# Kernel tuning notes

Measured on AMD Instinct MI355X. Metric: run time of the kernel, lower is better.

The kernel has to match this reference:

```python
import jax, jax.numpy as jnp
import numpy as np

B, N, K = 64, 128, 12
D_ATOM, D_NBR, D_NEW = 256, 320, 256
H, DK = 8, 32  # D_NEW = H * DK
LN_EPS = 1e-5
NEG_INF = -1e9


def setup_inputs() -> dict:
    key = jax.random.key(0)
    ks = jax.random.split(key, 10)
    atom_feature = jax.random.normal(ks[0], (B, N, D_ATOM), jnp.float32)
    atom_neighbor_feature = jax.random.normal(ks[1], (B, N, K, D_NBR), jnp.float32)
    # valid-neighbor masks from random neighbor counts in [1, K]
    counts = jax.random.randint(ks[2], (B, N), 1, K + 1)
    valid = (jnp.arange(K)[None, None, :] < counts[:, :, None]).astype(jnp.float32)
    atom_attend_mask = valid[..., None]                      # (B,N,K,1), 1=real neighbor
    atom_softmax_mask = (1.0 - valid[..., None]) * NEG_INF   # (B,N,K,1), additive
    # parameters
    s = 1.0 / np.sqrt(D_ATOM)
    W_atom = jax.random.uniform(ks[3], (D_ATOM, D_NEW), jnp.float32, -s, s)
    b_atom = jnp.zeros((D_NEW,), jnp.float32)
    s2 = 1.0 / np.sqrt(D_NBR)
    W_nbr = jax.random.uniform(ks[4], (D_NBR, D_NEW), jnp.float32, -s2, s2)
    b_nbr = jnp.zeros((D_NEW,), jnp.float32)
    s3 = 1.0 / np.sqrt(DK)
    w_align = jax.random.uniform(ks[5], (DK, 1), jnp.float32, -s3, s3)
    b_align = jnp.zeros((1,), jnp.float32)
    ln_gamma = jnp.ones((D_NEW,), jnp.float32)
    ln_beta = jnp.zeros((D_NEW,), jnp.float32)
    return dict(atom_feature=atom_feature, atom_neighbor_feature=atom_neighbor_feature,
                atom_softmax_mask=atom_softmax_mask, atom_attend_mask=atom_attend_mask,
                W_atom=W_atom, b_atom=b_atom, W_nbr=W_nbr, b_nbr=b_nbr,
                w_align=w_align, b_align=b_align, ln_gamma=ln_gamma, ln_beta=ln_beta)


def reference(atom_feature, atom_neighbor_feature, atom_softmax_mask, atom_attend_mask,
              W_atom, b_atom, W_nbr, b_nbr, w_align, b_align, ln_gamma, ln_beta):
    # dropout is identity at eval time
    h = atom_feature @ W_atom + b_atom                    # (B,N,D_NEW)
    e = atom_neighbor_feature @ W_nbr + b_nbr             # (B,N,K,D_NEW)
    h = h.reshape(B, N, 1, H, DK)                         # broadcast over K
    e = e.reshape(B, N, K, H, DK)
    # GATv2: act(h_i + e_j) then per-head linear score
    feat = jax.nn.leaky_relu(h + e)                       # slope 0.01 == torch default
    score = feat @ w_align + b_align                      # (B,N,K,H,1)
    score = score + atom_softmax_mask[:, :, :, None, :]   # additive -inf on pad
    attn = jax.nn.softmax(score, axis=2)                  # softmax over neighbors K
    attn = attn * atom_attend_mask[:, :, :, None, :]
    ctx = jnp.sum(attn * e, axis=2).reshape(B, N, H * DK)  # (B,N,D_NEW)
    # LayerNorm
    mu = jnp.mean(ctx, axis=-1, keepdims=True)
    xc = ctx - mu
    var = jnp.mean(xc * xc, axis=-1, keepdims=True)
    return xc * jax.lax.rsqrt(var + LN_EPS) * ln_gamma + ln_beta
```

## Files before the change

### kernel.cpp

```cpp
#include <hip/hip_runtime.h>

#define KN 12
#define DNBR 320
#define DNEW 256
#define BN_TOT 8192
#define ATB 4
#define KTOT 576
#define NKS 18
#define AROWS 55
#define ASTR 584

typedef short bf8_t __attribute__((ext_vector_type(8)));
typedef float f32x4 __attribute__((ext_vector_type(4)));
typedef unsigned short us8 __attribute__((ext_vector_type(8)));
using u16 = unsigned short;
using u32 = unsigned int;

__device__ __forceinline__ u16 f2bf(float f) {
    u32 x = __float_as_uint(f);
    return (u16)((x + 0x7fffu + ((x >> 16) & 1u)) >> 16);
}

__device__ __forceinline__ us8 pack8(float4 a, float4 b) {
    us8 v;
    v[0] = f2bf(a.x); v[1] = f2bf(a.y); v[2] = f2bf(a.z); v[3] = f2bf(a.w);
    v[4] = f2bf(b.x); v[5] = f2bf(b.y); v[6] = f2bf(b.z); v[7] = f2bf(b.w);
    return v;
}

__global__ __launch_bounds__(256) void build_b2(
    const float* __restrict__ Wn, const float* __restrict__ Wa,
    u16* __restrict__ B2)
{
    int tile = blockIdx.x * 4 + (threadIdx.x >> 6);
    int l = threadIdx.x & 63;
    int ks = tile >> 4, nt = tile & 15;
    int q = l >> 4, m = l & 15;
    int col = nt * 16 + m;
    us8 v;
#pragma unroll
    for (int e = 0; e < 8; e++) {
        int k = ks * 32 + q * 8 + e;
        float f = (k < DNBR) ? Wn[k * DNEW + col] : Wa[(k - DNBR) * DNEW + col];
        v[e] = f2bf(f);
    }
    *(us8*)&B2[(size_t)tile * 512 + l * 8] = v;
}

__global__ __launch_bounds__(256) void fused_all(
    const float* __restrict__ atomf, const float* __restrict__ nbrf,
    const float* __restrict__ smaskg, const float* __restrict__ amaskg,
    const float* __restrict__ ba, const u16* __restrict__ B2,
    const float* __restrict__ bnb, const float* __restrict__ walg,
    const float* __restrict__ balg, const float* __restrict__ gam,
    const float* __restrict__ bet, float* __restrict__ out)
{
    __shared__ u16 A[AROWS * ASTR];
    __shared__ float ctx_l[ATB][256];
    __shared__ float s_l[ATB][8][12];
    __shared__ float attnm_l[ATB][8][16];
    __shared__ float bias2_l[256], bnb_l[256], wal_l[32];
    __shared__ float smask_l[ATB * 12], amask_l[ATB * 12];
    __shared__ float red_l[ATB][8];

    const int t = threadIdx.x;
    const int l = t & 63, w = t >> 6, q = l >> 4, m = l & 15;
    const int a0 = blockIdx.x * ATB;

    bias2_l[t] = bnb[t] + ba[t];
    bnb_l[t] = bnb[t];
    if (t < 32) wal_l[t] = walg[t];
    if (t < 48) smask_l[t] = smaskg[(size_t)a0 * KN + t];
    if (t >= 64 && t < 112) amask_l[t - 64] = amaskg[(size_t)a0 * KN + (t - 64)];

    for (int idx = t; idx < AROWS * 72; idx += 256) {
        int R = idx / 72, c8 = idx - R * 72;
        int k0 = c8 * 8;
        us8 v = {0, 0, 0, 0, 0, 0, 0, 0};
        if (R < 52) {
            int at = R / 13, row = R - at * 13;
            const float* src = nullptr;
            if (row < 12) {
                if (k0 < DNBR) src = nbrf + ((size_t)(a0 + at) * KN + row) * DNBR + k0;
                else           src = atomf + (size_t)(a0 + at) * DNEW + (k0 - DNBR);
            } else if (k0 >= DNBR) {
                src = atomf + (size_t)(a0 + at) * DNEW + (k0 - DNBR);
            }
            if (src) v = pack8(*(const float4*)src, *(const float4*)(src + 4));
        }
        *(us8*)&A[R * ASTR + k0] = v;
    }
    __syncthreads();

    f32x4 acc[ATB][4];
#pragma unroll
    for (int at = 0; at < ATB; at++)
#pragma unroll
        for (int j = 0; j < 4; j++) acc[at][j] = (f32x4){0.f, 0.f, 0.f, 0.f};

    for (int ks = 0; ks < NKS; ks++) {
        bf8_t af[ATB], bf[4];
#pragma unroll
        for (int at = 0; at < ATB; at++)
            af[at] = *(bf8_t*)&A[(at * 13 + m) * ASTR + ks * 32 + q * 8];
#pragma unroll
        for (int j = 0; j < 4; j++)
            bf[j] = *(const bf8_t*)&B2[((size_t)(ks * 16 + w * 4 + j) * 64 + l) * 8];
#pragma unroll
        for (int at = 0; at < ATB; at++)
#pragma unroll
            for (int j = 0; j < 4; j++)
                acc[at][j] = __builtin_amdgcn_mfma_f32_16x16x32_bf16(af[at], bf[j], acc[at][j], 0, 0, 0);
    }

    const float bal = balg[0];
    float b2v[4], wv[4];
#pragma unroll
    for (int j = 0; j < 4; j++) {
        b2v[j] = bias2_l[w * 64 + j * 16 + m];
        wv[j] = wal_l[(j * 16 + m) & 31];
    }
#pragma unroll
    for (int at = 0; at < ATB; at++) {
#pragma unroll
        for (int jj = 0; jj < 2; jj++) {
#pragma unroll
            for (int r = 0; r < 4; r++) {
                float p = 0.f;
#pragma unroll
                for (int jo = 0; jo < 2; jo++) {
                    int j = jj * 2 + jo;
                    float f = acc[at][j][r] + b2v[j];
                    f = f > 0.f ? f : 0.01f * f;
                    p = fmaf(f, wv[j], p);
                }
                p += __shfl_xor(p, 1);
                p += __shfl_xor(p, 2);
                p += __shfl_xor(p, 4);
                p += __shfl_xor(p, 8);
                int k = q * 4 + r;
                if (m == 0 && k < 12)
                    s_l[at][w * 2 + jj][k] = p + bal + smask_l[at * 12 + k];
            }
        }
    }
    __syncthreads();

    if (t < 32) {
        int at = t >> 3, hd = t & 7;
        float sc[12], mx = -1e30f;
#pragma unroll
        for (int k = 0; k < 12; k++) { sc[k] = s_l[at][hd][k]; mx = fmaxf(mx, sc[k]); }
        float ss = 0.f;
#pragma unroll
        for (int k = 0; k < 12; k++) { sc[k] = __expf(sc[k] - mx); ss += sc[k]; }
        float inv = 1.f / ss;
        float sA = 0.f;
#pragma unroll
        for (int k = 0; k < 12; k++) {
            float a_ = sc[k] * inv * amask_l[at * 12 + k];
            attnm_l[at][hd][k] = a_;
            sA += a_;
        }
        attnm_l[at][hd][12] = -sA;
        attnm_l[at][hd][13] = 0.f;
        attnm_l[at][hd][14] = 0.f;
        attnm_l[at][hd][15] = 0.f;
    }
    __syncthreads();

#pragma unroll
    for (int at = 0; at < ATB; at++) {
#pragma unroll
        for (int j = 0; j < 4; j++) {
            int hd = w * 2 + (j >> 1);
            f32x4 am = *(f32x4*)&attnm_l[at][hd][q * 4];
            float cp = am[0] * acc[at][j][0] + am[1] * acc[at][j][1] +
                       am[2] * acc[at][j][2] + am[3] * acc[at][j][3];
            cp += __shfl_xor(cp, 16);
            cp += __shfl_xor(cp, 32);
            float sA = -attnm_l[at][hd][12];
            float cv = cp + sA * bnb_l[w * 64 + j * 16 + m];
            if (q == 0) ctx_l[at][w * 64 + j * 16 + m] = cv;
        }
    }
    __syncthreads();

    float x[ATB];
#pragma unroll
    for (int at = 0; at < ATB; at++) {
        x[at] = ctx_l[at][t];
        float s1 = x[at], s2 = x[at] * x[at];
#pragma unroll
        for (int off = 1; off < 64; off <<= 1) {
            s1 += __shfl_xor(s1, off);
            s2 += __shfl_xor(s2, off);
        }
        if (l == 0) { red_l[at][w] = s1; red_l[at][4 + w] = s2; }
    }
    __syncthreads();
#pragma unroll
    for (int at = 0; at < ATB; at++) {
        float ts1 = red_l[at][0] + red_l[at][1] + red_l[at][2] + red_l[at][3];
        float ts2 = red_l[at][4] + red_l[at][5] + red_l[at][6] + red_l[at][7];
        float mu = ts1 * (1.f / 256.f);
        float var = ts2 * (1.f / 256.f) - mu * mu;
        var = fmaxf(var, 0.f);
        float r = rsqrtf(var + 1e-5f);
        out[(size_t)(a0 + at) * DNEW + t] = (x[at] - mu) * r * gam[t] + bet[t];
    }
}

extern "C" void kernel_launch(void* const* d_in, const int* in_sizes, int n_in,
                              void* d_out, int out_size, void* d_ws, size_t ws_size,
                              hipStream_t stream) {
    const float* atomf = (const float*)d_in[0];
    const float* nbrf  = (const float*)d_in[1];
    const float* smask = (const float*)d_in[2];
    const float* amask = (const float*)d_in[3];
    const float* Wa    = (const float*)d_in[4];
    const float* ba    = (const float*)d_in[5];
    const float* Wn    = (const float*)d_in[6];
    const float* bnb   = (const float*)d_in[7];
    const float* wal   = (const float*)d_in[8];
    const float* bal   = (const float*)d_in[9];
    const float* gam   = (const float*)d_in[10];
    const float* bet   = (const float*)d_in[11];
    float* outp = (float*)d_out;

    u16* B2 = (u16*)d_ws;

    build_b2<<<72, 256, 0, stream>>>(Wn, Wa, B2);
    fused_all<<<BN_TOT / ATB, 256, 0, stream>>>(atomf, nbrf, smask, amask, ba,
                                                B2, bnb, wal, bal, gam, bet, outp);
}
```

Measured before the change: 291.5 us.

## Split atom and neighbor projections into separate GEMMs with two atoms per block

Computes the atom projection once per atom in a small separate MFMA loop instead of concatenating atom features onto every neighbor row. This removes the redundant K-dimension work and lets the neighbor bias be added directly, which simplifies the context correction. Each block now handles two atoms instead of four, with a smaller LDS footprint and a launch bound targeting higher occupancy. The cost is that weight tiles are reloaded from global memory twice as often per atom.

```diff
diff --git a/kernel.cpp b/kernel.cpp
--- a/kernel.cpp
+++ b/kernel.cpp
@@ -4,11 +4,11 @@
 #define DNBR 320
 #define DNEW 256
 #define BN_TOT 8192
-#define ATB 4
-#define KTOT 576
-#define NKS 18
-#define AROWS 55
-#define ASTR 584
+#define ATB 2
+#define NKS_E 10
+#define NKS_H 8
+#define ASTR_E 328
+#define ASTR_H 264
 
 typedef short bf8_t __attribute__((ext_vector_type(8)));
 typedef float f32x4 __attribute__((ext_vector_type(4)));
@@ -34,20 +34,26 @@
 {
     int tile = blockIdx.x * 4 + (threadIdx.x >> 6);
     int l = threadIdx.x & 63;
-    int ks = tile >> 4, nt = tile & 15;
     int q = l >> 4, m = l & 15;
-    int col = nt * 16 + m;
     us8 v;
-#pragma unroll
-    for (int e = 0; e < 8; e++) {
-        int k = ks * 32 + q * 8 + e;
-        float f = (k < DNBR) ? Wn[k * DNEW + col] : Wa[(k - DNBR) * DNEW + col];
-        v[e] = f2bf(f);
+    if (tile < 160) {
+        int ks = tile >> 4, nt = tile & 15;
+        int col = nt * 16 + m;
+#pragma unroll
+        for (int e = 0; e < 8; e++)
+            v[e] = f2bf(Wn[(ks * 32 + q * 8 + e) * DNEW + col]);
+    } else {
+        int tt = tile - 160;
+        int ks = tt >> 4, nt = tt & 15;
+        int col = nt * 16 + m;
+#pragma unroll
+        for (int e = 0; e < 8; e++)
+            v[e] = f2bf(Wa[(ks * 32 + q * 8 + e) * DNEW + col]);
     }
     *(us8*)&B2[(size_t)tile * 512 + l * 8] = v;
 }
 
-__global__ __launch_bounds__(256) void fused_all(
+__global__ __launch_bounds__(256, 4) void fused_all(
     const float* __restrict__ atomf, const float* __restrict__ nbrf,
     const float* __restrict__ smaskg, const float* __restrict__ amaskg,
     const float* __restrict__ ba, const u16* __restrict__ B2,
@@ -55,11 +61,13 @@
     const float* __restrict__ balg, const float* __restrict__ gam,
     const float* __restrict__ bet, float* __restrict__ out)
 {
-    __shared__ u16 A[AROWS * ASTR];
+    __shared__ u16 A_e[32 * ASTR_E];
+    __shared__ u16 A_h[16 * ASTR_H];
+    __shared__ float h_l[ATB][256];
     __shared__ float ctx_l[ATB][256];
     __shared__ float s_l[ATB][8][12];
     __shared__ float attnm_l[ATB][8][16];
-    __shared__ float bias2_l[256], bnb_l[256], wal_l[32];
+    __shared__ float bnb_l[256], ba_l[256], wal_l[32];
     __shared__ float smask_l[ATB * 12], amask_l[ATB * 12];
     __shared__ float red_l[ATB][8];
 
@@ -67,58 +75,94 @@
     const int l = t & 63, w = t >> 6, q = l >> 4, m = l & 15;
     const int a0 = blockIdx.x * ATB;
 
-    bias2_l[t] = bnb[t] + ba[t];
     bnb_l[t] = bnb[t];
+    ba_l[t] = ba[t];
     if (t < 32) wal_l[t] = walg[t];
-    if (t < 48) smask_l[t] = smaskg[(size_t)a0 * KN + t];
-    if (t >= 64 && t < 112) amask_l[t - 64] = amaskg[(size_t)a0 * KN + (t - 64)];
-
-    for (int idx = t; idx < AROWS * 72; idx += 256) {
-        int R = idx / 72, c8 = idx - R * 72;
-        int k0 = c8 * 8;
-        us8 v = {0, 0, 0, 0, 0, 0, 0, 0};
-        if (R < 52) {
-            int at = R / 13, row = R - at * 13;
-            const float* src = nullptr;
-            if (row < 12) {
-                if (k0 < DNBR) src = nbrf + ((size_t)(a0 + at) * KN + row) * DNBR + k0;
-                else           src = atomf + (size_t)(a0 + at) * DNEW + (k0 - DNBR);
-            } else if (k0 >= DNBR) {
-                src = atomf + (size_t)(a0 + at) * DNEW + (k0 - DNBR);
-            }
-            if (src) v = pack8(*(const float4*)src, *(const float4*)(src + 4));
-        }
-        *(us8*)&A[R * ASTR + k0] = v;
-    }
-    __syncthreads();
-
-    f32x4 acc[ATB][4];
+    else if (t >= 32 && t < 56) smask_l[t - 32] = smaskg[(size_t)a0 * KN + (t - 32)];
+    else if (t >= 64 && t < 88) amask_l[t - 64] = amaskg[(size_t)a0 * KN + (t - 64)];
+
+    const float* nbase = nbrf + (size_t)a0 * (KN * DNBR);
+    for (int i = t; i < 960; i += 256) {
+        float4 v0 = *(const float4*)(nbase + i * 8);
+        float4 v1 = *(const float4*)(nbase + i * 8 + 4);
+        int at = i / 480, rem = i - at * 480;
+        int row = rem / 40, c8 = rem - row * 40;
+        *(us8*)&A_e[(at * 16 + row) * ASTR_E + c8 * 8] = pack8(v0, v1);
+    }
+    for (int i = t; i < 328; i += 256) {
+        int at = i / 164, rem = i - at * 164;
+        int rr = rem / 41, c8 = rem - rr * 41;
+        us8 z = {0, 0, 0, 0, 0, 0, 0, 0};
+        *(us8*)&A_e[(at * 16 + 12 + rr) * ASTR_E + c8 * 8] = z;
+    }
+    if (t < 64) {
+        int at = t >> 5, c8 = t & 31;
+        const float* s = atomf + (size_t)(a0 + at) * DNEW + c8 * 8;
+        *(us8*)&A_h[at * ASTR_H + c8 * 8] = pack8(*(const float4*)s, *(const float4*)(s + 4));
+    }
+    for (int i = t; i < 462; i += 256) {
+        int rr = i / 33, c8 = i - rr * 33;
+        us8 z = {0, 0, 0, 0, 0, 0, 0, 0};
+        *(us8*)&A_h[(2 + rr) * ASTR_H + c8 * 8] = z;
+    }
+    __syncthreads();
+
+    f32x4 acc_e[ATB][4];
+    f32x4 acc_h[4];
 #pragma unroll
     for (int at = 0; at < ATB; at++)
 #pragma unroll
-        for (int j = 0; j < 4; j++) acc[at][j] = (f32x4){0.f, 0.f, 0.f, 0.f};
-
-    for (int ks = 0; ks < NKS; ks++) {
-        bf8_t af[ATB], bf[4];
-#pragma unroll
-        for (int at = 0; at < ATB; at++)
-            af[at] = *(bf8_t*)&A[(at * 13 + m) * ASTR + ks * 32 + q * 8];
+        for (int j = 0; j < 4; j++) acc_e[at][j] = (f32x4){0.f, 0.f, 0.f, 0.f};
+#pragma unroll
+    for (int j = 0; j < 4; j++) acc_h[j] = (f32x4){0.f, 0.f, 0.f, 0.f};
+
+    for (int ks = 0; ks < NKS_E; ks++) {
+        bf8_t af0 = *(bf8_t*)&A_e[(0 * 16 + m) * ASTR_E + ks * 32 + q * 8];
+        bf8_t af1 = *(bf8_t*)&A_e[(1 * 16 + m) * ASTR_E + ks * 32 + q * 8];
+        bf8_t bf[4];
 #pragma unroll
         for (int j = 0; j < 4; j++)
             bf[j] = *(const bf8_t*)&B2[((size_t)(ks * 16 + w * 4 + j) * 64 + l) * 8];
 #pragma unroll
+        for (int j = 0; j < 4; j++) {
+            acc_e[0][j] = __builtin_amdgcn_mfma_f32_16x16x32_bf16(af0, bf[j], acc_e[0][j], 0, 0, 0);
+            acc_e[1][j] = __builtin_amdgcn_mfma_f32_16x16x32_bf16(af1, bf[j], acc_e[1][j], 0, 0, 0);
+        }
+    }
+    for (int ks = 0; ks < NKS_H; ks++) {
+        bf8_t af = *(bf8_t*)&A_h[m * ASTR_H + ks * 32 + q * 8];
+#pragma unroll
+        for (int j = 0; j < 4; j++) {
+            bf8_t bfj = *(const bf8_t*)&B2[((size_t)(160 + ks * 16 + w * 4 + j) * 64 + l) * 8];
+            acc_h[j] = __builtin_amdgcn_mfma_f32_16x16x32_bf16(af, bfj, acc_h[j], 0, 0, 0);
+        }
+    }
+    if (q == 0) {
+#pragma unroll
+        for (int j = 0; j < 4; j++) {
+            int col = w * 64 + j * 16 + m;
+            h_l[0][col] = acc_h[j][0] + ba_l[col];
+            h_l[1][col] = acc_h[j][1] + ba_l[col];
+        }
+    }
+    __syncthreads();
+
+#pragma unroll
+    for (int j = 0; j < 4; j++) {
+        float bv = bnb_l[w * 64 + j * 16 + m];
+#pragma unroll
         for (int at = 0; at < ATB; at++)
 #pragma unroll
-            for (int j = 0; j < 4; j++)
-                acc[at][j] = __builtin_amdgcn_mfma_f32_16x16x32_bf16(af[at], bf[j], acc[at][j], 0, 0, 0);
+            for (int r = 0; r < 4; r++) acc_e[at][j][r] += bv;
     }
 
     const float bal = balg[0];
-    float b2v[4], wv[4];
+    float hv[ATB][4], wv[4];
 #pragma unroll
     for (int j = 0; j < 4; j++) {
-        b2v[j] = bias2_l[w * 64 + j * 16 + m];
         wv[j] = wal_l[(j * 16 + m) & 31];
+#pragma unroll
+        for (int at = 0; at < ATB; at++) hv[at][j] = h_l[at][w * 64 + j * 16 + m];
     }
 #pragma unroll
     for (int at = 0; at < ATB; at++) {
@@ -130,7 +174,7 @@
 #pragma unroll
                 for (int jo = 0; jo < 2; jo++) {
                     int j = jj * 2 + jo;
-                    float f = acc[at][j][r] + b2v[j];
+                    float f = acc_e[at][j][r] + hv[at][j];
                     f = f > 0.f ? f : 0.01f * f;
                     p = fmaf(f, wv[j], p);
                 }
@@ -146,7 +190,7 @@
     }
     __syncthreads();
 
-    if (t < 32) {
+    if (t < ATB * 8) {
         int at = t >> 3, hd = t & 7;
         float sc[12], mx = -1e30f;
 #pragma unroll
@@ -155,14 +199,10 @@
 #pragma unroll
         for (int k = 0; k < 12; k++) { sc[k] = __expf(sc[k] - mx); ss += sc[k]; }
         float inv = 1.f / ss;
-        float sA = 0.f;
-#pragma unroll
-        for (int k = 0; k < 12; k++) {
-            float a_ = sc[k] * inv * amask_l[at * 12 + k];
-            attnm_l[at][hd][k] = a_;
-            sA += a_;
-        }
-        attnm_l[at][hd][12] = -sA;
+#pragma unroll
+        for (int k = 0; k < 12; k++)
+            attnm_l[at][hd][k] = sc[k] * inv * amask_l[at * 12 + k];
+        attnm_l[at][hd][12] = 0.f;
         attnm_l[at][hd][13] = 0.f;
         attnm_l[at][hd][14] = 0.f;
         attnm_l[at][hd][15] = 0.f;
@@ -175,13 +215,11 @@
         for (int j = 0; j < 4; j++) {
             int hd = w * 2 + (j >> 1);
             f32x4 am = *(f32x4*)&attnm_l[at][hd][q * 4];
-            float cp = am[0] * acc[at][j][0] + am[1] * acc[at][j][1] +
-                       am[2] * acc[at][j][2] + am[3] * acc[at][j][3];
+            float cp = am[0] * acc_e[at][j][0] + am[1] * acc_e[at][j][1] +
+                       am[2] * acc_e[at][j][2] + am[3] * acc_e[at][j][3];
             cp += __shfl_xor(cp, 16);
             cp += __shfl_xor(cp, 32);
-            float sA = -attnm_l[at][hd][12];
-            float cv = cp + sA * bnb_l[w * 64 + j * 16 + m];
-            if (q == 0) ctx_l[at][w * 64 + j * 16 + m] = cv;
+            if (q == 0) ctx_l[at][w * 64 + j * 16 + m] = cp;
         }
     }
     __syncthreads();
```

Measured after the change: 268.0 us. -8.0%, faster.
